# Kernel optimization log

Measured on AMD Instinct MI355X. Metric: run time of the kernel, lower is better.

Reference implementation:

```python
import jax, jax.numpy as jnp
import numpy as np

B, S, H = 2, 8192, 1024
NUM_HEADS = 16
HEAD_DIM = H // NUM_HEADS
KERNEL = 7
DILATION = 1
SCALE = 1.0 / np.sqrt(HEAD_DIM)


def setup_inputs() -> dict:
    key = jax.random.key(0)
    ks = jax.random.split(key, 9)
    init = 0.02
    return {
        "hidden_states": jax.random.normal(ks[0], (B, S, H), dtype=jnp.float32),
        "w_q": jax.random.normal(ks[1], (H, H), dtype=jnp.float32) * init,
        "b_q": jnp.zeros((H,), dtype=jnp.float32),
        "w_k": jax.random.normal(ks[2], (H, H), dtype=jnp.float32) * init,
        "b_k": jnp.zeros((H,), dtype=jnp.float32),
        "w_v": jax.random.normal(ks[3], (H, H), dtype=jnp.float32) * init,
        "b_v": jnp.zeros((H,), dtype=jnp.float32),
        "w_o": jax.random.normal(ks[4], (H, H), dtype=jnp.float32) * init,
        "b_o": jnp.zeros((H,), dtype=jnp.float32),
    }


def reference(hidden_states, w_q, b_q, w_k, b_k, w_v, b_v, w_o, b_o):
    b, s, h = hidden_states.shape
    # QKV projections (weights stored [in, out])
    q = hidden_states @ w_q + b_q
    k = hidden_states @ w_k + b_k
    v = hidden_states @ w_v + b_v
    # [B, nH, S, hd]
    q = q.reshape(b, s, NUM_HEADS, HEAD_DIM).transpose(0, 2, 1, 3)
    k = k.reshape(b, s, NUM_HEADS, HEAD_DIM).transpose(0, 2, 1, 3)
    v = v.reshape(b, s, NUM_HEADS, HEAD_DIM).transpose(0, 2, 1, 3)

    # Neighborhood window indices: for query i, keys at i + (j - K//2)*dilation
    offsets = (jnp.arange(KERNEL) - KERNEL // 2) * DILATION  # [K]
    idx = jnp.arange(s)[:, None] + offsets[None, :]          # [S, K]
    valid = (idx >= 0) & (idx < s)                           # [S, K]
    idx_c = jnp.clip(idx, 0, s - 1)

    k_win = k[:, :, idx_c, :]  # [B, nH, S, K, hd]
    v_win = v[:, :, idx_c, :]  # [B, nH, S, K, hd]

    scores = jnp.einsum('bhsd,bhskd->bhsk', q, k_win) * SCALE
    scores = jnp.where(valid[None, None], scores, -jnp.inf)
    attn = jax.nn.softmax(scores, axis=-1)                   # [B, nH, S, K]
    out = jnp.einsum('bhsk,bhskd->bhsd', attn, v_win)        # [B, nH, S, hd]

    out = out.transpose(0, 2, 1, 3).reshape(b, s, h)
    return out @ w_o + b_o
```

## Files before the change

kernel.cpp:

```cpp
#include <hip/hip_runtime.h>


typedef __bf16 bf16x8 __attribute__((ext_vector_type(8)));
typedef float f32x4 __attribute__((ext_vector_type(4)));
typedef int int4v __attribute__((ext_vector_type(4)));
typedef unsigned short u16x8 __attribute__((ext_vector_type(8)));
typedef __attribute__((address_space(1))) void as1_void;
typedef __attribute__((address_space(3))) void as3_void;

__device__ __forceinline__ float bf2f(unsigned short u) {
    union { unsigned int u; float f; } c;
    c.u = ((unsigned int)u) << 16;
    return c.f;
}
__device__ __forceinline__ unsigned short f2bf(float f) {
    union { float f; unsigned int u; } c;
    c.f = f;
    unsigned int u = c.u;
    u += 0x7fffu + ((u >> 16) & 1u);
    return (unsigned short)(u >> 16);
}

__global__ __launch_bounds__(256) void prep(
    const float* __restrict__ X, const float* __restrict__ w0,
    const float* __restrict__ w1, const float* __restrict__ w2,
    const float* __restrict__ w3, const float* __restrict__ bq,
    const float* __restrict__ bk, const float* __restrict__ bv,
    unsigned short* __restrict__ Xb, unsigned short* __restrict__ t0,
    unsigned short* __restrict__ t3, float* __restrict__ biasQ) {
    __shared__ unsigned short tile[32][33];
    const int bid = blockIdx.x;
    if (bid < 16384) {
        int i = bid * 256 + threadIdx.x;
        float4 v = ((const float4*)X)[i];
        ushort4 o;
        o.x = f2bf(v.x); o.y = f2bf(v.y); o.z = f2bf(v.z); o.w = f2bf(v.w);
        ((ushort4*)Xb)[i] = o;
    } else if (bid < 20480) {
        const int t = bid - 16384;
        const int z = t >> 10;
        const int rem = t & 1023;
        const float* W = (z == 0) ? w0 : (z == 1) ? w1 : (z == 2) ? w2 : w3;
        unsigned short* Wt = (z == 3) ? t3 : t0 + (size_t)z * 1048576;
        const int c0 = (rem & 31) * 32;
        const int r0 = (rem >> 5) * 32;
        const int tx = threadIdx.x & 31;
        const int ty = threadIdx.x >> 5;
#pragma unroll
        for (int i = 0; i < 32; i += 8)
            tile[ty + i][tx] = f2bf(W[(size_t)(r0 + ty + i) * 1024 + c0 + tx]);
        __syncthreads();
#pragma unroll
        for (int i = 0; i < 32; i += 8)
            Wt[(size_t)(c0 + ty + i) * 1024 + r0 + tx] = tile[tx][ty + i];
    } else {
        int i = (bid - 20480) * 256 + threadIdx.x;
        if (i < 3072)
            biasQ[i] = (i < 1024) ? bq[i] : ((i < 2048) ? bk[i - 1024] : bv[i - 2048]);
    }
}

__global__ __launch_bounds__(512, 2) void gemm_qkv8(
    const unsigned short* __restrict__ A, const unsigned short* __restrict__ Bt,
    const float* __restrict__ bias, unsigned short* __restrict__ Cb) {
    constexpr int K = 1024;
    constexpr int NT = 16;
    __shared__ unsigned short smem[65536];
    const int tid  = threadIdx.x;
    const int lane = tid & 63;
    const int wave = tid >> 6;
    const int quad = lane >> 4;
    const int mr   = lane & 15;

    const int id  = blockIdx.x;
    const int swz = (id & 7) * 96 + (id >> 3);
    const int bm  = (swz / 12) * 256;
    const int bn  = (swz % 12) * 256;
    const int wm  = (wave >> 2) * 128;
    const int wn  = (wave & 3) * 64;

    const int r0 = tid >> 3;
    const int g8 = ((lane & 7) ^ ((lane >> 3) & 7)) * 8;
    const unsigned short* srcA = A  + (size_t)(bm + r0) * K + g8;
    const unsigned short* srcB = Bt + (size_t)(bn + r0) * K + g8;

    auto stage = [&](const unsigned short* gb, int ldsByte, int kt) {
#pragma unroll
        for (int l = 0; l < 2; ++l)
            __builtin_amdgcn_global_load_lds(
                (const as1_void*)(gb + (size_t)l * 65536 + kt),
                (as3_void*)((char*)smem + ldsByte + l * 8192 + tid * 16),
                16, 0, 0);
    };

    stage(srcA,          0,     0);
    stage(srcA + 131072, 16384, 0);
    stage(srcB,          32768, 0);
    stage(srcB + 131072, 49152, 0);
    stage(srcB,          65536 + 32768, 64);
    stage(srcB + 131072, 65536 + 49152, 64);
    asm volatile("s_waitcnt vmcnt(4)" ::: "memory");
    asm volatile("s_barrier" ::: "memory");

    const int aRow = (wm + mr) * 64;
    const int bRow = 16384 + (wn + mr) * 64;
    const int c8_0 = ((0 * 4 + quad) ^ (mr & 7)) * 8;
    const int c8_1 = ((1 * 4 + quad) ^ (mr & 7)) * 8;

    f32x4 acc[8][4] = {};

    for (int t = 0; t < NT; ++t) {
        const int bufS  = (t & 1) << 15;
        const int nbufB = ((t + 1) & 1) << 16;
        const int cbufB = (t & 1) << 16;
        const int ktA = (t + 1 < NT ? t + 1 : NT - 1) * 64;
        const int ktB = (t + 2 < NT ? t + 2 : NT - 1) * 64;

        bf16x8 afL[4][2], bA[2][2], bB[2][2];
#pragma unroll
        for (int i = 0; i < 4; ++i) {
            afL[i][0] = *(const bf16x8*)(smem + bufS + aRow + i * 1024 + c8_0);
            afL[i][1] = *(const bf16x8*)(smem + bufS + aRow + i * 1024 + c8_1);
        }
#pragma unroll
        for (int j = 0; j < 2; ++j) {
            bA[j][0] = *(const bf16x8*)(smem + bufS + bRow + j * 1024 + c8_0);
            bA[j][1] = *(const bf16x8*)(smem + bufS + bRow + j * 1024 + c8_1);
        }
#pragma unroll
        for (int j = 0; j < 2; ++j) {
            bB[j][0] = *(const bf16x8*)(smem + bufS + bRow + (j + 2) * 1024 + c8_0);
            bB[j][1] = *(const bf16x8*)(smem + bufS + bRow + (j + 2) * 1024 + c8_1);
        }
        stage(srcA, nbufB, ktA);
        __builtin_amdgcn_s_setprio(1);
#pragma unroll
        for (int i = 0; i < 4; ++i)
#pragma unroll
            for (int j = 0; j < 2; ++j) {
                acc[i][j] = __builtin_amdgcn_mfma_f32_16x16x32_bf16(afL[i][0], bA[j][0], acc[i][j], 0, 0, 0);
                acc[i][j] = __builtin_amdgcn_mfma_f32_16x16x32_bf16(afL[i][1], bA[j][1], acc[i][j], 0, 0, 0);
            }
        __builtin_amdgcn_s_setprio(0);
        asm volatile("s_barrier" ::: "memory");

        stage(srcA + 131072, nbufB + 16384, ktA);
        __builtin_amdgcn_s_setprio(1);
#pragma unroll
        for (int i = 0; i < 4; ++i)
#pragma unroll
            for (int j = 0; j < 2; ++j) {
                acc[i][j + 2] = __builtin_amdgcn_mfma_f32_16x16x32_bf16(afL[i][0], bB[j][0], acc[i][j + 2], 0, 0, 0);
                acc[i][j + 2] = __builtin_amdgcn_mfma_f32_16x16x32_bf16(afL[i][1], bB[j][1], acc[i][j + 2], 0, 0, 0);
            }
        __builtin_amdgcn_s_setprio(0);
        asm volatile("s_barrier" ::: "memory");

        bf16x8 afH[4][2];
#pragma unroll
        for (int i = 0; i < 4; ++i) {
            afH[i][0] = *(const bf16x8*)(smem + bufS + aRow + (i + 4) * 1024 + c8_0);
            afH[i][1] = *(const bf16x8*)(smem + bufS + aRow + (i + 4) * 1024 + c8_1);
        }
        stage(srcB, cbufB + 32768, ktB);
        __builtin_amdgcn_s_setprio(1);
#pragma unroll
        for (int i = 0; i < 4; ++i)
#pragma unroll
            for (int j = 0; j < 2; ++j) {
                acc[i + 4][j + 2] = __builtin_amdgcn_mfma_f32_16x16x32_bf16(afH[i][0], bB[j][0], acc[i + 4][j + 2], 0, 0, 0);
                acc[i + 4][j + 2] = __builtin_amdgcn_mfma_f32_16x16x32_bf16(afH[i][1], bB[j][1], acc[i + 4][j + 2], 0, 0, 0);
            }
        __builtin_amdgcn_s_setprio(0);
        asm volatile("s_barrier" ::: "memory");

        stage(srcB + 131072, cbufB + 49152, ktB);
        __builtin_amdgcn_s_setprio(1);
#pragma unroll
        for (int i = 0; i < 4; ++i)
#pragma unroll
            for (int j = 0; j < 2; ++j) {
                acc[i + 4][j] = __builtin_amdgcn_mfma_f32_16x16x32_bf16(afH[i][0], bA[j][0], acc[i + 4][j], 0, 0, 0);
                acc[i + 4][j] = __builtin_amdgcn_mfma_f32_16x16x32_bf16(afH[i][1], bA[j][1], acc[i + 4][j], 0, 0, 0);
            }
        __builtin_amdgcn_s_setprio(0);
        asm volatile("s_waitcnt vmcnt(4)" ::: "memory");
        asm volatile("s_barrier" ::: "memory");
    }

    asm volatile("s_waitcnt vmcnt(0) lgkmcnt(0)" ::: "memory");
    asm volatile("s_barrier" ::: "memory");

    unsigned short* ep = smem + wave * 8192;
#pragma unroll
    for (int h = 0; h < 2; ++h) {
#pragma unroll
        for (int j = 0; j < 4; ++j) {
            const float bvv = bias[bn + wn + j * 16 + mr];
#pragma unroll
            for (int i = 0; i < 4; ++i)
#pragma unroll
                for (int r = 0; r < 4; ++r)
                    ep[(i * 16 + quad * 4 + r) * 68 + j * 16 + mr] =
                        f2bf(acc[h * 4 + i][j][r] + bvv);
        }
#pragma unroll
        for (int p = 0; p < 8; ++p) {
            const int row = p * 8 + (lane >> 3);
            const int gr = lane & 7;
            int4v v = *(const int4v*)(ep + row * 68 + gr * 8);
            *(int4v*)(Cb + (size_t)(bm + wm + h * 64 + row) * 3072 + bn + wn + gr * 8) = v;
        }
    }
}

__global__ __launch_bounds__(256) void attn_wave(
    const unsigned short* __restrict__ QKV, unsigned short* __restrict__ out) {
    const int lane = threadIdx.x & 63;
    const int wv   = threadIdx.x >> 6;
    const int tok  = blockIdx.x * 4 + wv;
    const int s    = tok & 8191;
    const size_t rowQ = (size_t)tok * 3072;
    const int le8 = lane * 8;

    float qf0[8], qf1[8];
    {
        u16x8 a = *(const u16x8*)(QKV + rowQ + le8);
        u16x8 b = *(const u16x8*)(QKV + rowQ + 512 + le8);
#pragma unroll
        for (int e = 0; e < 8; ++e) { qf0[e] = bf2f(a[e]); qf1[e] = bf2f(b[e]); }
    }

    float sc0[7], sc1[7];
#pragma unroll
    for (int j = 0; j < 7; ++j) {
        const int ks = s + j - 3;
        const bool ok = (ks >= 0) & (ks < 8192);
        const int kc = ks < 0 ? 0 : (ks > 8191 ? 8191 : ks);
        const size_t kb = rowQ + (size_t)(kc - s) * 3072 + 1024;
        u16x8 k0 = *(const u16x8*)(QKV + kb + le8);
        u16x8 k1 = *(const u16x8*)(QKV + kb + 512 + le8);
        float d0 = 0.f, d1 = 0.f;
#pragma unroll
        for (int e = 0; e < 8; ++e) {
            d0 += qf0[e] * bf2f(k0[e]);
            d1 += qf1[e] * bf2f(k1[e]);
        }
#pragma unroll
        for (int off = 1; off <= 4; off <<= 1) {
            d0 += __shfl_xor(d0, off);
            d1 += __shfl_xor(d1, off);
        }
        sc0[j] = ok ? d0 * 0.125f : -__builtin_inff();
        sc1[j] = ok ? d1 * 0.125f : -__builtin_inff();
    }

    float mx0 = sc0[0], mx1 = sc1[0];
#pragma unroll
    for (int j = 1; j < 7; ++j) { mx0 = fmaxf(mx0, sc0[j]); mx1 = fmaxf(mx1, sc1[j]); }
    float p0[7], p1[7], sum0 = 0.f, sum1 = 0.f;
#pragma unroll
    for (int j = 0; j < 7; ++j) {
        p0[j] = __builtin_amdgcn_exp2f((sc0[j] - mx0) * 1.44269504f);
        p1[j] = __builtin_amdgcn_exp2f((sc1[j] - mx1) * 1.44269504f);
        sum0 += p0[j]; sum1 += p1[j];
    }
    const float inv0 = __builtin_amdgcn_rcpf(sum0);
    const float inv1 = __builtin_amdgcn_rcpf(sum1);

    float o0[8] = {}, o1[8] = {};
#pragma unroll
    for (int j = 0; j < 7; ++j) {
        const int ks = s + j - 3;
        const int kc = ks < 0 ? 0 : (ks > 8191 ? 8191 : ks);
        const size_t vb = rowQ + (size_t)(kc - s) * 3072 + 2048;
        u16x8 v0 = *(const u16x8*)(QKV + vb + le8);
        u16x8 v1 = *(const u16x8*)(QKV + vb + 512 + le8);
        const float w0 = p0[j] * inv0;
        const float w1 = p1[j] * inv1;
#pragma unroll
        for (int e = 0; e < 8; ++e) {
            o0[e] += w0 * bf2f(v0[e]);
            o1[e] += w1 * bf2f(v1[e]);
        }
    }

    const size_t dst = (size_t)tok * 1024;
    u16x8 s0v, s1v;
#pragma unroll
    for (int e = 0; e < 8; ++e) { s0v[e] = f2bf(o0[e]); s1v[e] = f2bf(o1[e]); }
    *(u16x8*)(out + dst + le8) = s0v;
    *(u16x8*)(out + dst + 512 + le8) = s1v;
}

template <int MODE, int MT>
__device__ __forceinline__ void gemm_body(
    const unsigned short* __restrict__ A, const unsigned short* __restrict__ Bt,
    const float* __restrict__ bias, float* __restrict__ Cf,
    int N, int K) {
    __shared__ unsigned short smem[MT * 2048 + 8192];
    const int tid = threadIdx.x;
    const int lane = tid & 63;
    const int wave = tid >> 6;
    const int bm = blockIdx.y * (MT * 32);
    const int bn = blockIdx.x * 128;
    const int wm = (wave >> 1) * (MT * 16);
    const int wn = (wave & 1) * 64;
    const int quad = lane >> 4;
    const int mr = lane & 15;

    const unsigned short* gA[MT];
    const unsigned short* gB[4];
    char* lA[MT];
    char* lB[4];
#pragma unroll
    for (int k = 0; k < MT; ++k) {
        const int q = (k * 4 + wave) * 64 + lane;
        const int row = q >> 3;
        const int c8 = (q & 7) ^ (row & 7);
        gA[k] = A + (size_t)(bm + row) * K + c8 * 8;
        lA[k] = (char*)smem + (size_t)(k * 4 + wave) * 1024;
    }
#pragma unroll
    for (int k = 0; k < 4; ++k) {
        const int q = (k * 4 + wave) * 64 + lane;
        const int row = q >> 3;
        const int c8 = (q & 7) ^ (row & 7);
        gB[k] = Bt + (size_t)(bn + row) * K + c8 * 8;
        lB[k] = (char*)smem + (size_t)MT * 4096 + (size_t)(k * 4 + wave) * 1024;
    }

    f32x4 acc[MT][4] = {};

    for (int kt = 0; kt < K; kt += 64) {
#pragma unroll
        for (int k = 0; k < MT; ++k) {
            __builtin_amdgcn_global_load_lds((as1_void*)gA[k], (as3_void*)lA[k], 16, 0, 0);
            gA[k] += 64;
        }
#pragma unroll
        for (int k = 0; k < 4; ++k) {
            __builtin_amdgcn_global_load_lds((as1_void*)gB[k], (as3_void*)lB[k], 16, 0, 0);
            gB[k] += 64;
        }
        __syncthreads();

#pragma unroll
        for (int kk = 0; kk < 2; ++kk) {
            const int c8 = (kk * 4 + quad) ^ (mr & 7);
            bf16x8 af[MT], bfr[4];
#pragma unroll
            for (int i = 0; i < MT; ++i)
                af[i] = *(const bf16x8*)(smem + (wm + i * 16 + mr) * 64 + c8 * 8);
#pragma unroll
            for (int j = 0; j < 4; ++j)
                bfr[j] = *(const bf16x8*)(smem + MT * 2048 + (wn + j * 16 + mr) * 64 + c8 * 8);
#pragma unroll
            for (int i = 0; i < MT; ++i)
#pragma unroll
                for (int j = 0; j < 4; ++j)
                    acc[i][j] = __builtin_amdgcn_mfma_f32_16x16x32_bf16(
                        af[i], bfr[j], acc[i][j], 0, 0, 0);
        }
        __syncthreads();
    }

    if (MODE == 0) {
        float* epf = (float*)smem + wave * 1280;
#pragma unroll
        for (int j = 0; j < 4; ++j) {
            const int gcol0 = bn + wn + j * 16;
            const float bv = bias[gcol0 + mr];
#pragma unroll
            for (int h2 = 0; h2 < MT / 4; ++h2) {
#pragma unroll
                for (int i2 = 0; i2 < 4; ++i2)
#pragma unroll
                    for (int r = 0; r < 4; ++r)
                        epf[(i2 * 16 + quad * 4 + r) * 20 + mr] = acc[h2 * 4 + i2][j][r] + bv;
#pragma unroll
                for (int p = 0; p < 4; ++p) {
                    const int dr = p * 16 + (lane >> 2);
                    const int ch = lane & 3;
                    f32x4 v = *(const f32x4*)(epf + dr * 20 + ch * 4);
                    *(f32x4*)(Cf + (size_t)(bm + wm + h2 * 64 + dr) * N + gcol0 + ch * 4) = v;
                }
            }
        }
    }
}

__global__ __launch_bounds__(256, 4) void gemm_out(
    const unsigned short* __restrict__ A, const unsigned short* __restrict__ Bt,
    const float* __restrict__ bias, float* __restrict__ Cf, int N, int K) {
    gemm_body<0, 4>(A, Bt, bias, Cf, N, K);
}

extern "C" void kernel_launch(void* const* d_in, const int* in_sizes, int n_in,
                              void* d_out, int out_size, void* d_ws, size_t ws_size,
                              hipStream_t stream) {
    (void)in_sizes; (void)n_in; (void)out_size; (void)ws_size;
    const float* X  = (const float*)d_in[0];
    const float* wq = (const float*)d_in[1];
    const float* bq = (const float*)d_in[2];
    const float* wk = (const float*)d_in[3];
    const float* bk = (const float*)d_in[4];
    const float* wv = (const float*)d_in[5];
    const float* bv = (const float*)d_in[6];
    const float* wo = (const float*)d_in[7];
    const float* bo = (const float*)d_in[8];
    float* out = (float*)d_out;

    char* ws = (char*)d_ws;
    unsigned short* Xb    = (unsigned short*)(ws);
    unsigned short* WtQKV = (unsigned short*)(ws + 33554432);
    unsigned short* WtO   = (unsigned short*)(ws + 39845888);
    unsigned short* QKV   = (unsigned short*)(ws + 41943040);
    unsigned short* AttnO = (unsigned short*)(ws + 142606336);
    float*          biasQ = (float*)(ws + 176160768);

    prep<<<20492, 256, 0, stream>>>(X, wq, wk, wv, wo, bq, bk, bv,
                                    Xb, WtQKV, WtO, biasQ);

    gemm_qkv8<<<768, 512, 0, stream>>>(Xb, WtQKV, biasQ, QKV);

    attn_wave<<<4096, 256, 0, stream>>>(QKV, AttnO);

    gemm_out<<<dim3(8, 128), 256, 0, stream>>>(AttnO, WtO, bo, out, 1024, 1024);
}
```

Measured before the change: 326.1 us.

## Process four consecutive tokens per wave to reuse K/V rows across windows

Each wave now handles four adjacent query tokens and loads the 10 K and V rows covering their combined 7-wide windows once, instead of 7 rows per token. This cuts redundant global/L2 loads of K and V by sharing them across overlapping windows. The block index is also swizzled so consecutive blocks land on different positions in the sequence. In exchange, register use per thread rises (scores, weights and accumulators for four tokens), which may lower occupancy, and the grid shrinks to a quarter of the blocks.

```diff
diff --git a/kernel.cpp b/kernel.cpp
--- a/kernel.cpp
+++ b/kernel.cpp
@@ -214,83 +214,109 @@
     }
 }
 
-__global__ __launch_bounds__(256) void attn_wave(
+__global__ __launch_bounds__(256) void attn_wave4(
     const unsigned short* __restrict__ QKV, unsigned short* __restrict__ out) {
     const int lane = threadIdx.x & 63;
     const int wv   = threadIdx.x >> 6;
-    const int tok  = blockIdx.x * 4 + wv;
-    const int s    = tok & 8191;
-    const size_t rowQ = (size_t)tok * 3072;
-    const int le8 = lane * 8;
-
-    float qf0[8], qf1[8];
-    {
-        u16x8 a = *(const u16x8*)(QKV + rowQ + le8);
-        u16x8 b = *(const u16x8*)(QKV + rowQ + 512 + le8);
-#pragma unroll
-        for (int e = 0; e < 8; ++e) { qf0[e] = bf2f(a[e]); qf1[e] = bf2f(b[e]); }
-    }
-
-    float sc0[7], sc1[7];
-#pragma unroll
-    for (int j = 0; j < 7; ++j) {
-        const int ks = s + j - 3;
-        const bool ok = (ks >= 0) & (ks < 8192);
+    const int id   = blockIdx.x;
+    const int swz  = (id & 7) * 128 + (id >> 3);
+    const int tok0 = swz * 16 + wv * 4;
+    const int s0   = tok0 & 8191;
+    const int bb   = tok0 - s0;
+    const int le8  = lane * 8;
+
+    const float NEG = -__builtin_inff();
+
+    u16x8 qa[4][2];
+#pragma unroll
+    for (int t = 0; t < 4; ++t) {
+        const size_t rq = (size_t)(tok0 + t) * 3072;
+        qa[t][0] = *(const u16x8*)(QKV + rq + le8);
+        qa[t][1] = *(const u16x8*)(QKV + rq + 512 + le8);
+    }
+
+    float sc0[4][7], sc1[4][7];
+#pragma unroll
+    for (int ri = 0; ri < 10; ++ri) {
+        const int ks = s0 + ri - 3;
+        const bool okr = (ks >= 0) & (ks < 8192);
         const int kc = ks < 0 ? 0 : (ks > 8191 ? 8191 : ks);
-        const size_t kb = rowQ + (size_t)(kc - s) * 3072 + 1024;
+        const size_t kb = (size_t)(bb + kc) * 3072 + 1024;
         u16x8 k0 = *(const u16x8*)(QKV + kb + le8);
         u16x8 k1 = *(const u16x8*)(QKV + kb + 512 + le8);
-        float d0 = 0.f, d1 = 0.f;
-#pragma unroll
-        for (int e = 0; e < 8; ++e) {
-            d0 += qf0[e] * bf2f(k0[e]);
-            d1 += qf1[e] * bf2f(k1[e]);
-        }
-#pragma unroll
-        for (int off = 1; off <= 4; off <<= 1) {
-            d0 += __shfl_xor(d0, off);
-            d1 += __shfl_xor(d1, off);
-        }
-        sc0[j] = ok ? d0 * 0.125f : -__builtin_inff();
-        sc1[j] = ok ? d1 * 0.125f : -__builtin_inff();
-    }
-
-    float mx0 = sc0[0], mx1 = sc1[0];
-#pragma unroll
-    for (int j = 1; j < 7; ++j) { mx0 = fmaxf(mx0, sc0[j]); mx1 = fmaxf(mx1, sc1[j]); }
-    float p0[7], p1[7], sum0 = 0.f, sum1 = 0.f;
-#pragma unroll
-    for (int j = 0; j < 7; ++j) {
-        p0[j] = __builtin_amdgcn_exp2f((sc0[j] - mx0) * 1.44269504f);
-        p1[j] = __builtin_amdgcn_exp2f((sc1[j] - mx1) * 1.44269504f);
-        sum0 += p0[j]; sum1 += p1[j];
-    }
-    const float inv0 = __builtin_amdgcn_rcpf(sum0);
-    const float inv1 = __builtin_amdgcn_rcpf(sum1);
-
-    float o0[8] = {}, o1[8] = {};
-#pragma unroll
-    for (int j = 0; j < 7; ++j) {
-        const int ks = s + j - 3;
+#pragma unroll
+        for (int t = 0; t < 4; ++t) {
+            const int j = ri - t;
+            if (j >= 0 && j < 7) {
+                float d0 = 0.f, d1 = 0.f;
+#pragma unroll
+                for (int e = 0; e < 8; ++e) {
+                    d0 += bf2f(qa[t][0][e]) * bf2f(k0[e]);
+                    d1 += bf2f(qa[t][1][e]) * bf2f(k1[e]);
+                }
+#pragma unroll
+                for (int off = 1; off <= 4; off <<= 1) {
+                    d0 += __shfl_xor(d0, off);
+                    d1 += __shfl_xor(d1, off);
+                }
+                sc0[t][j] = okr ? d0 * 0.125f : NEG;
+                sc1[t][j] = okr ? d1 * 0.125f : NEG;
+            }
+        }
+    }
+
+    float w0[4][7], w1[4][7];
+#pragma unroll
+    for (int t = 0; t < 4; ++t) {
+        float mx0 = sc0[t][0], mx1 = sc1[t][0];
+#pragma unroll
+        for (int j = 1; j < 7; ++j) { mx0 = fmaxf(mx0, sc0[t][j]); mx1 = fmaxf(mx1, sc1[t][j]); }
+        float s0s = 0.f, s1s = 0.f;
+#pragma unroll
+        for (int j = 0; j < 7; ++j) {
+            w0[t][j] = __builtin_amdgcn_exp2f((sc0[t][j] - mx0) * 1.44269504f);
+            w1[t][j] = __builtin_amdgcn_exp2f((sc1[t][j] - mx1) * 1.44269504f);
+            s0s += w0[t][j]; s1s += w1[t][j];
+        }
+        const float i0 = __builtin_amdgcn_rcpf(s0s);
+        const float i1 = __builtin_amdgcn_rcpf(s1s);
+#pragma unroll
+        for (int j = 0; j < 7; ++j) { w0[t][j] *= i0; w1[t][j] *= i1; }
+    }
+
+    float o0[4][8] = {}, o1[4][8] = {};
+#pragma unroll
+    for (int ri = 0; ri < 10; ++ri) {
+        const int ks = s0 + ri - 3;
         const int kc = ks < 0 ? 0 : (ks > 8191 ? 8191 : ks);
-        const size_t vb = rowQ + (size_t)(kc - s) * 3072 + 2048;
+        const size_t vb = (size_t)(bb + kc) * 3072 + 2048;
         u16x8 v0 = *(const u16x8*)(QKV + vb + le8);
         u16x8 v1 = *(const u16x8*)(QKV + vb + 512 + le8);
-        const float w0 = p0[j] * inv0;
-        const float w1 = p1[j] * inv1;
-#pragma unroll
-        for (int e = 0; e < 8; ++e) {
-            o0[e] += w0 * bf2f(v0[e]);
-            o1[e] += w1 * bf2f(v1[e]);
-        }
-    }
-
-    const size_t dst = (size_t)tok * 1024;
-    u16x8 s0v, s1v;
-#pragma unroll
-    for (int e = 0; e < 8; ++e) { s0v[e] = f2bf(o0[e]); s1v[e] = f2bf(o1[e]); }
-    *(u16x8*)(out + dst + le8) = s0v;
-    *(u16x8*)(out + dst + 512 + le8) = s1v;
+        float vf0[8], vf1[8];
+#pragma unroll
+        for (int e = 0; e < 8; ++e) { vf0[e] = bf2f(v0[e]); vf1[e] = bf2f(v1[e]); }
+#pragma unroll
+        for (int t = 0; t < 4; ++t) {
+            const int j = ri - t;
+            if (j >= 0 && j < 7) {
+#pragma unroll
+                for (int e = 0; e < 8; ++e) {
+                    o0[t][e] += w0[t][j] * vf0[e];
+                    o1[t][e] += w1[t][j] * vf1[e];
+                }
+            }
+        }
+    }
+
+#pragma unroll
+    for (int t = 0; t < 4; ++t) {
+        const size_t dst = (size_t)(tok0 + t) * 1024;
+        u16x8 a, b2;
+#pragma unroll
+        for (int e = 0; e < 8; ++e) { a[e] = f2bf(o0[t][e]); b2[e] = f2bf(o1[t][e]); }
+        *(u16x8*)(out + dst + le8) = a;
+        *(u16x8*)(out + dst + 512 + le8) = b2;
+    }
 }
 
 template <int MODE, int MT>
@@ -424,7 +450,7 @@
 
     gemm_qkv8<<<768, 512, 0, stream>>>(Xb, WtQKV, biasQ, QKV);
 
-    attn_wave<<<4096, 256, 0, stream>>>(QKV, AttnO);
+    attn_wave4<<<1024, 256, 0, stream>>>(QKV, AttnO);
 
     gemm_out<<<dim3(8, 128), 256, 0, stream>>>(AttnO, WtO, bo, out, 1024, 1024);
 }
```

Measured after the change: 327.7 us. No clear change (+0.5%).
